# Performance work log

Hardware: AMD Instinct MI355X
Metric: run time of the kernel (lower is better)

## Reference

```python
import jax, jax.numpy as jnp
import numpy as np


def setup_inputs() -> dict:
    key = jax.random.key(0)
    ks = jax.random.split(key, 12)
    B, T, n, m = 128, 64, 81, 128
    inp = {
        "X": jax.random.normal(ks[0], (B, T, n), dtype=jnp.float32),
        "h0": jax.random.normal(ks[1], (B, m), dtype=jnp.float32),
        "s0": jax.random.normal(ks[2], (B, m), dtype=jnp.float32),
        "W_lstm": jax.random.normal(ks[3], (n, 4 * m), dtype=jnp.float32) * 0.05,
        "U_lstm": jax.random.normal(ks[4], (m, 4 * m), dtype=jnp.float32) * 0.05,
        "b_lstm": jax.random.normal(ks[5], (4 * m,), dtype=jnp.float32) * 0.05,
        "We_w": jax.random.normal(ks[6], (2 * m, T), dtype=jnp.float32) * 0.05,
        "We_b": jax.random.normal(ks[7], (T,), dtype=jnp.float32) * 0.05,
        "Ue_w": jax.random.normal(ks[8], (T, T), dtype=jnp.float32) * 0.05,
        "Ue_b": jax.random.normal(ks[9], (T,), dtype=jnp.float32) * 0.05,
        "ve_w": jax.random.normal(ks[10], (T, 1), dtype=jnp.float32) * 0.05,
        "ve_b": jax.random.normal(ks[11], (1,), dtype=jnp.float32) * 0.05,
    }
    return inp


def reference(X, h0, s0, W_lstm, U_lstm, b_lstm, We_w, We_b, Ue_w, Ue_b, ve_w, ve_b):
    # Faithful to the TF code: initial_state=[h0, s0] is re-passed at every t,
    # so each timestep is an INDEPENDENT single LSTM cell step from (h0, s0).
    # This lets us vectorize the whole Python loop over t.
    B, T, n = X.shape
    m = h0.shape[1]
    # gates for all timesteps at once: (B, T, 4m). Keras gate order: i, f, g(c), o.
    gates = jnp.einsum('btn,ng->btg', X, W_lstm) + (h0 @ U_lstm + b_lstm)[:, None, :]
    i = jax.nn.sigmoid(gates[..., 0 * m:1 * m])
    f = jax.nn.sigmoid(gates[..., 1 * m:2 * m])
    g = jnp.tanh(gates[..., 2 * m:3 * m])
    o = jax.nn.sigmoid(gates[..., 3 * m:4 * m])
    c = f * s0[:, None, :] + i * g          # (B, T, m)
    h = o * jnp.tanh(c)                     # (B, T, m)
    # Input attention, vectorized over t.
    hc = jnp.concatenate([h, c], axis=-1)   # (B, T, 2m)
    A = hc @ We_w + We_b                    # (B, T, T)  = W_e([h;c]) per step t
    U = jnp.einsum('btn,tk->bnk', X, Ue_w) + Ue_b  # (B, n, T) = U_e(X^T)
    # e[b,t,i] = v_e(tanh(A[b,t,:] + U[b,i,:]))
    e = jnp.tanh(A[:, :, None, :] + U[:, None, :, :])       # (B, T, n, T)
    scores = jnp.einsum('btnk,k->btn', e, ve_w[:, 0]) + ve_b[0]  # (B, T, n)
    alpha = jax.nn.softmax(scores, axis=-1)                 # (B, T, n)
    # stack() gives (T, B, 1, n); tf.multiply broadcasts with X (B, T, n) -> (T, B, T, n)
    out = X[None, :, :, :] * jnp.transpose(alpha, (1, 0, 2))[:, :, None, :]
    return out
```

## Files before the change

### kernel.cpp

```cpp
#include <hip/hip_runtime.h>
#include <math.h>

#define BB 128
#define TT_ 64
#define NN 81
#define MM 128
#define GG 512
#define TN 5184
#define TCH 8
#define NBLK2 (BB * (TT_ / TCH))
#define SC_ 2.8853900817779268f

__device__ __forceinline__ float sigmoidf_(float x) {
    return 1.0f / (1.0f + __expf(-x));
}
__device__ __forceinline__ float fast_tanh(float x) {
    float e = __expf(2.0f * x);
    return 1.0f - 2.0f / (e + 1.0f);
}

__global__ __launch_bounds__(256) void k1_prep(
    const float* __restrict__ X, const float* __restrict__ h0,
    const float* __restrict__ U_lstm, const float* __restrict__ b_lstm,
    const float* __restrict__ Ue_w, const float* __restrict__ Ue_b,
    float* __restrict__ ws_hb, float* __restrict__ ws_U)
{
    __shared__ float Xl[TN];
    __shared__ float sUe[64 * 16];
    __shared__ float h0l[MM];

    int blk = blockIdx.x;
    int b = blk >> 2;
    int q = blk & 3;
    int tid = threadIdx.x;

    for (int p = tid; p < TN; p += 256) Xl[p] = X[b * TN + p];
    for (int p = tid; p < 1024; p += 256) {
        int t = p >> 4, kl = p & 15;
        sUe[p] = Ue_w[t * TT_ + q * 16 + kl];
    }
    if (q == 0 && tid < MM) h0l[tid] = h0[b * MM + tid];
    __syncthreads();

    if (q == 0) {
        float2 bl = ((const float2*)b_lstm)[tid];
        float a0 = bl.x, a1 = bl.y;
        for (int j = 0; j < MM; ++j) {
            float h = h0l[j];
            float2 w = ((const float2*)&U_lstm[j * GG])[tid];
            a0 += h * w.x;
            a1 += h * w.y;
        }
        ((float2*)&ws_hb[b * GG])[tid] = make_float2(a0, a1);
    }

    int kl = tid & 15;
    int k  = q * 16 + kl;
    int ir = tid >> 4;
    float ueb = Ue_b[k];
#pragma unroll
    for (int pass = 0; pass < 6; ++pass) {
        int i = pass * 16 + ir;
        if (i < NN) {
            float acc = ueb;
#pragma unroll 8
            for (int t = 0; t < TT_; ++t)
                acc += Xl[t * NN + i] * sUe[t * 16 + kl];
            ws_U[b * TN + i * 64 + k] = acc * SC_;
        }
    }
}

__global__ __launch_bounds__(256, 4) void k2_main(
    const float* __restrict__ X, const float* __restrict__ s0,
    const float* __restrict__ W_lstm,
    const float* __restrict__ We_w, const float* __restrict__ We_b,
    const float* __restrict__ ve_w, const float* __restrict__ ve_b,
    const float* __restrict__ ws_hb, const float* __restrict__ ws_U,
    float* __restrict__ out)
{
    __shared__ alignas(16) float sXct[NN * TCH];
    __shared__ float sU[NN * 65];
    __shared__ float sHc[TCH * 256];
    __shared__ float sA[TCH * 65];
    __shared__ float sSc[TCH * NN];
    __shared__ float sVe[TT_];

    int blk = blockIdx.x;
    int b  = blk >> 3;
    int tc = blk & 7;
    int t0 = tc * TCH;
    int tid = threadIdx.x;
    int u    = tid & 127;
    int half = tid >> 7;
    float veb = ve_b[0];

    float hb0 = ws_hb[b * GG + u];
    float hb1 = ws_hb[b * GG + 128 + u];
    float hb2 = ws_hb[b * GG + 256 + u];
    float hb3 = ws_hb[b * GG + 384 + u];
    float s0v = s0[b * MM + u];

    for (int p = tid; p < NN * TCH; p += 256) {
        float v = X[b * TN + t0 * NN + p];
        int tt = p / NN, np = p - tt * NN;
        sXct[np * TCH + tt] = v;
    }
    for (int p = tid; p < TN; p += 256) {
        int i = p >> 6, k = p & 63;
        sU[i * 65 + k] = ws_U[b * TN + p];
    }
    if (tid < TT_) sVe[tid] = ve_w[tid];
    __syncthreads();

    float acc[4][4];
#pragma unroll
    for (int r = 0; r < 4; ++r) {
        acc[r][0] = hb0; acc[r][1] = hb1; acc[r][2] = hb2; acc[r][3] = hb3;
    }
    {
        const float* Wl = &W_lstm[u];
        for (int n = 0; n < NN; ++n) {
            float w0 = Wl[n * GG];
            float w1 = Wl[n * GG + 128];
            float w2 = Wl[n * GG + 256];
            float w3 = Wl[n * GG + 384];
            float4 xv = *(const float4*)&sXct[n * TCH + 4 * half];
            acc[0][0] += xv.x * w0; acc[0][1] += xv.x * w1; acc[0][2] += xv.x * w2; acc[0][3] += xv.x * w3;
            acc[1][0] += xv.y * w0; acc[1][1] += xv.y * w1; acc[1][2] += xv.y * w2; acc[1][3] += xv.y * w3;
            acc[2][0] += xv.z * w0; acc[2][1] += xv.z * w1; acc[2][2] += xv.z * w2; acc[2][3] += xv.z * w3;
            acc[3][0] += xv.w * w0; acc[3][1] += xv.w * w1; acc[3][2] += xv.w * w2; acc[3][3] += xv.w * w3;
        }
    }
#pragma unroll
    for (int r = 0; r < 4; ++r) {
        int tt = 4 * half + r;
        float gi = sigmoidf_(acc[r][0]);
        float gf = sigmoidf_(acc[r][1]);
        float gg = fast_tanh(acc[r][2]);
        float go = sigmoidf_(acc[r][3]);
        float c  = gf * s0v + gi * gg;
        float h  = go * fast_tanh(c);
        sHc[tt * 256 + u]       = h;
        sHc[tt * 256 + 128 + u] = c;
    }
    __syncthreads();

    int wv = tid >> 6;
    int l  = tid & 63;

    {
        float a0 = We_b[l], a1 = a0;
        const float* Wep = &We_w[l];
        for (int j = 0; j < 256; ++j) {
            float w  = Wep[j * TT_];
            a0 += sHc[wv * 256 + j]       * w;
            a1 += sHc[(wv + 4) * 256 + j] * w;
        }
        sA[wv * 65 + l]       = a0 * SC_;
        sA[(wv + 4) * 65 + l] = a1 * SC_;
    }
    float sumVe;
    {
        float sv = sVe[l];
        sumVe = sv;
        for (int d = 32; d >= 1; d >>= 1) sumVe += __shfl_xor(sumVe, d, 64);
    }

#pragma unroll
    for (int hh = 0; hh < 2; ++hh) {
        int tt = wv + hh * 4;
        const float* Ar = &sA[tt * 65];
        float sc0, sc1;
        {
            const float* Ur = &sU[l * 65];
            float a2 = 0.f;
#pragma unroll 8
            for (int k = 0; k < TT_; ++k) {
                float s = Ar[k] + Ur[k];
                float e = exp2f(s);
                float r2 = __builtin_amdgcn_rcpf(e + 1.0f);
                a2 = fmaf(sVe[k], r2, a2);
            }
            sc0 = sumVe - 2.0f * a2 + veb;
        }
        bool v2 = (l + 64 < NN);
        if (v2) {
            const float* Ur = &sU[(l + 64) * 65];
            float a2 = 0.f;
#pragma unroll 8
            for (int k = 0; k < TT_; ++k) {
                float s = Ar[k] + Ur[k];
                float e = exp2f(s);
                float r2 = __builtin_amdgcn_rcpf(e + 1.0f);
                a2 = fmaf(sVe[k], r2, a2);
            }
            sc1 = sumVe - 2.0f * a2 + veb;
        } else {
            sc1 = -1e30f;
        }
        float mx = fmaxf(sc0, sc1);
        for (int d = 32; d >= 1; d >>= 1) mx = fmaxf(mx, __shfl_xor(mx, d, 64));
        float ea = __expf(sc0 - mx);
        float eb = v2 ? __expf(sc1 - mx) : 0.f;
        float s = ea + eb;
        for (int d = 32; d >= 1; d >>= 1) s += __shfl_xor(s, d, 64);
        float inv = 1.f / s;
        sSc[tt * NN + l] = ea * inv;
        if (v2) sSc[tt * NN + l + 64] = eb * inv;
    }
    __syncthreads();

    {
        const float* Xb = &X[b * TN];
        for (int j = tid; j < TN; j += 256) {
            float x = Xb[j];
            int i = j % NN;
#pragma unroll
            for (int tt = 0; tt < TCH; ++tt) {
                out[((size_t)(t0 + tt) * BB + b) * TN + j] = x * sSc[tt * NN + i];
            }
        }
    }
}

extern "C" void kernel_launch(void* const* d_in, const int* in_sizes, int n_in,
                              void* d_out, int out_size, void* d_ws, size_t ws_size,
                              hipStream_t stream) {
    const float* X      = (const float*)d_in[0];
    const float* h0     = (const float*)d_in[1];
    const float* s0     = (const float*)d_in[2];
    const float* W_lstm = (const float*)d_in[3];
    const float* U_lstm = (const float*)d_in[4];
    const float* b_lstm = (const float*)d_in[5];
    const float* We_w   = (const float*)d_in[6];
    const float* We_b   = (const float*)d_in[7];
    const float* Ue_w   = (const float*)d_in[8];
    const float* Ue_b   = (const float*)d_in[9];
    const float* ve_w   = (const float*)d_in[10];
    const float* ve_b   = (const float*)d_in[11];
    float* out = (float*)d_out;

    float* ws    = (float*)d_ws;
    float* ws_hb = ws;
    float* ws_U  = ws + BB * GG;

    k1_prep<<<BB * 4, 256, 0, stream>>>(X, h0, U_lstm, b_lstm, Ue_w, Ue_b, ws_hb, ws_U);
    k2_main<<<NBLK2, 256, 0, stream>>>(X, s0, W_lstm, We_w, We_b, ve_w, ve_b,
                                       ws_hb, ws_U, out);
}
```

Measured before the change: 249.2 us.

## Split output broadcast into separate kernel with vectorized nontemporal stores

Moves the large output-write stage (X times alpha, 5184 floats written for each of 8 timesteps per block) out of the attention kernel into a dedicated third kernel. Alpha is passed through a global workspace buffer. The new kernel loads X as float4 and writes the output with 128-bit nontemporal stores. This is meant to stop the compute-heavy attention kernel's occupancy from limiting write bandwidth, at the cost of an extra launch and a small round trip of alpha through global memory.

```diff
diff --git a/kernel.cpp b/kernel.cpp
--- a/kernel.cpp
+++ b/kernel.cpp
@@ -11,6 +11,8 @@
 #define NBLK2 (BB * (TT_ / TCH))
 #define SC_ 2.8853900817779268f
 
+typedef float f32x4 __attribute__((ext_vector_type(4)));
+
 __device__ __forceinline__ float sigmoidf_(float x) {
     return 1.0f / (1.0f + __expf(-x));
 }
@@ -71,19 +73,18 @@
     }
 }
 
-__global__ __launch_bounds__(256, 4) void k2_main(
+__global__ __launch_bounds__(256, 4) void k2_attn(
     const float* __restrict__ X, const float* __restrict__ s0,
     const float* __restrict__ W_lstm,
     const float* __restrict__ We_w, const float* __restrict__ We_b,
     const float* __restrict__ ve_w, const float* __restrict__ ve_b,
     const float* __restrict__ ws_hb, const float* __restrict__ ws_U,
-    float* __restrict__ out)
+    float* __restrict__ ws_al)
 {
     __shared__ alignas(16) float sXct[NN * TCH];
     __shared__ float sU[NN * 65];
     __shared__ float sHc[TCH * 256];
     __shared__ float sA[TCH * 65];
-    __shared__ float sSc[TCH * NN];
     __shared__ float sVe[TT_];
 
     int blk = blockIdx.x;
@@ -206,20 +207,47 @@
         float s = ea + eb;
         for (int d = 32; d >= 1; d >>= 1) s += __shfl_xor(s, d, 64);
         float inv = 1.f / s;
-        sSc[tt * NN + l] = ea * inv;
-        if (v2) sSc[tt * NN + l + 64] = eb * inv;
-    }
-    __syncthreads();
-
-    {
-        const float* Xb = &X[b * TN];
-        for (int j = tid; j < TN; j += 256) {
-            float x = Xb[j];
-            int i = j % NN;
-#pragma unroll
-            for (int tt = 0; tt < TCH; ++tt) {
-                out[((size_t)(t0 + tt) * BB + b) * TN + j] = x * sSc[tt * NN + i];
-            }
+        float* alr = &ws_al[((size_t)b * TT_ + (t0 + tt)) * NN];
+        alr[l] = ea * inv;
+        if (v2) alr[l + 64] = eb * inv;
+    }
+}
+
+#define TPB3 8
+__global__ __launch_bounds__(256) void k3_out(
+    const float* __restrict__ X, const float* __restrict__ ws_al,
+    float* __restrict__ out)
+{
+    __shared__ float sAl[TPB3 * NN];
+    int blk = blockIdx.x;
+    int b  = blk >> 3;
+    int tg = blk & 7;
+    int t0 = tg * TPB3;
+    int tid = threadIdx.x;
+
+    for (int p = tid; p < TPB3 * NN; p += 256)
+        sAl[p] = ws_al[((size_t)b * TT_ + t0) * NN + p];
+    __syncthreads();
+
+    const f32x4* Xb4 = (const f32x4*)(X + (size_t)b * TN);
+    f32x4* out4 = (f32x4*)out;
+
+    for (int p = tid; p < TN / 4; p += 256) {
+        f32x4 x4 = Xb4[p];
+        int j = p * 4;
+        int i0 = j % NN;
+        int i1 = i0 + 1; if (i1 == NN) i1 = 0;
+        int i2 = i1 + 1; if (i2 == NN) i2 = 0;
+        int i3 = i2 + 1; if (i3 == NN) i3 = 0;
+#pragma unroll
+        for (int tt = 0; tt < TPB3; ++tt) {
+            const float* al = &sAl[tt * NN];
+            f32x4 o;
+            o.x = x4.x * al[i0];
+            o.y = x4.y * al[i1];
+            o.z = x4.z * al[i2];
+            o.w = x4.w * al[i3];
+            __builtin_nontemporal_store(o, out4 + ((size_t)(t0 + tt) * BB + b) * (TN / 4) + p);
         }
     }
 }
@@ -244,8 +272,10 @@
     float* ws    = (float*)d_ws;
     float* ws_hb = ws;
     float* ws_U  = ws + BB * GG;
+    float* ws_al = ws + BB * GG + BB * TN;
 
     k1_prep<<<BB * 4, 256, 0, stream>>>(X, h0, U_lstm, b_lstm, Ue_w, Ue_b, ws_hb, ws_U);
-    k2_main<<<NBLK2, 256, 0, stream>>>(X, s0, W_lstm, We_w, We_b, ve_w, ve_b,
-                                       ws_hb, ws_U, out);
-}
+    k2_attn<<<NBLK2, 256, 0, stream>>>(X, s0, W_lstm, We_w, We_b, ve_w, ve_b,
+                                       ws_hb, ws_U, ws_al);
+    k3_out<<<BB * (TT_ / TPB3), 256, 0, stream>>>(X, ws_al, out);
+}
```

Result: slower. 275.1 us (+10.4%).

## Factor exp of attention sum into product, vectorize per-wave output writes

Applied to the files above, without the earlier changes.

The score loop now precomputes exp2 of the A and U terms separately, so the inner loop does a multiply instead of an exp2 per element, using exp(a+b)=exp(a)exp(b). The final output stage is restructured so each wave writes its own two timesteps with float4 nontemporal stores, and the block barrier is replaced by an LDS waitcnt, since each wave only reads softmax rows it wrote itself. Risks are overflow or underflow in the factored exponentials, and relying on wave-local data ownership for correctness without the barrier.

```diff
diff --git a/kernel.cpp b/kernel.cpp
--- a/kernel.cpp
+++ b/kernel.cpp
@@ -11,6 +11,8 @@
 #define NBLK2 (BB * (TT_ / TCH))
 #define SC_ 2.8853900817779268f
 
+typedef float f32x4 __attribute__((ext_vector_type(4)));
+
 __device__ __forceinline__ float sigmoidf_(float x) {
     return 1.0f / (1.0f + __expf(-x));
 }
@@ -66,7 +68,7 @@
 #pragma unroll 8
             for (int t = 0; t < TT_; ++t)
                 acc += Xl[t * NN + i] * sUe[t * 16 + kl];
-            ws_U[b * TN + i * 64 + k] = acc * SC_;
+            ws_U[b * TN + i * 64 + k] = exp2f(acc * SC_);
         }
     }
 }
@@ -157,8 +159,8 @@
             a0 += sHc[wv * 256 + j]       * w;
             a1 += sHc[(wv + 4) * 256 + j] * w;
         }
-        sA[wv * 65 + l]       = a0 * SC_;
-        sA[(wv + 4) * 65 + l] = a1 * SC_;
+        sA[wv * 65 + l]       = exp2f(a0 * SC_);
+        sA[(wv + 4) * 65 + l] = exp2f(a1 * SC_);
     }
     float sumVe;
     {
@@ -166,6 +168,8 @@
         sumVe = sv;
         for (int d = 32; d >= 1; d >>= 1) sumVe += __shfl_xor(sumVe, d, 64);
     }
+    asm volatile("s_waitcnt lgkmcnt(0)" ::: "memory");
+    __builtin_amdgcn_sched_barrier(0);
 
 #pragma unroll
     for (int hh = 0; hh < 2; ++hh) {
@@ -177,8 +181,7 @@
             float a2 = 0.f;
 #pragma unroll 8
             for (int k = 0; k < TT_; ++k) {
-                float s = Ar[k] + Ur[k];
-                float e = exp2f(s);
+                float e = Ar[k] * Ur[k];
                 float r2 = __builtin_amdgcn_rcpf(e + 1.0f);
                 a2 = fmaf(sVe[k], r2, a2);
             }
@@ -190,8 +193,7 @@
             float a2 = 0.f;
 #pragma unroll 8
             for (int k = 0; k < TT_; ++k) {
-                float s = Ar[k] + Ur[k];
-                float e = exp2f(s);
+                float e = Ar[k] * Ur[k];
                 float r2 = __builtin_amdgcn_rcpf(e + 1.0f);
                 a2 = fmaf(sVe[k], r2, a2);
             }
@@ -209,17 +211,29 @@
         sSc[tt * NN + l] = ea * inv;
         if (v2) sSc[tt * NN + l + 64] = eb * inv;
     }
-    __syncthreads();
-
-    {
-        const float* Xb = &X[b * TN];
-        for (int j = tid; j < TN; j += 256) {
-            float x = Xb[j];
-            int i = j % NN;
-#pragma unroll
-            for (int tt = 0; tt < TCH; ++tt) {
-                out[((size_t)(t0 + tt) * BB + b) * TN + j] = x * sSc[tt * NN + i];
-            }
+    asm volatile("s_waitcnt lgkmcnt(0)" ::: "memory");
+    __builtin_amdgcn_sched_barrier(0);
+
+    {
+        const f32x4* Xb4 = (const f32x4*)(X + (size_t)b * TN);
+        f32x4* o0 = (f32x4*)out + ((size_t)(t0 + wv)     * BB + b) * (TN / 4);
+        f32x4* o1 = (f32x4*)out + ((size_t)(t0 + wv + 4) * BB + b) * (TN / 4);
+        const float* al0 = &sSc[wv * NN];
+        const float* al1 = &sSc[(wv + 4) * NN];
+        int i0 = (4 * l) % NN;
+        for (int p = l; p < TN / 4; p += 64) {
+            f32x4 x4 = Xb4[p];
+            int i1 = i0 + 1; if (i1 >= NN) i1 -= NN;
+            int i2 = i1 + 1; if (i2 >= NN) i2 -= NN;
+            int i3 = i2 + 1; if (i3 >= NN) i3 -= NN;
+            f32x4 oa, ob;
+            oa.x = x4.x * al0[i0]; oa.y = x4.y * al0[i1];
+            oa.z = x4.z * al0[i2]; oa.w = x4.w * al0[i3];
+            ob.x = x4.x * al1[i0]; ob.y = x4.y * al1[i1];
+            ob.z = x4.z * al1[i2]; ob.w = x4.w * al1[i3];
+            __builtin_nontemporal_store(oa, o0 + p);
+            __builtin_nontemporal_store(ob, o1 + p);
+            i0 += 13; if (i0 >= NN) i0 -= NN;
         }
     }
 }
```

Result: slower. 255.5 us (+2.5%).
